# Kernel optimization log

Hardware: AMD Instinct MI355X
Metric: run time of the kernel (lower is better)

The kernel has to match this reference:

```python
import jax, jax.numpy as jnp
import numpy as np
from jax.ops import segment_sum

N_NODES = 50000
N_EDGES = 800000
D = 128
N_LAYERS = 3
N_GRAPHS = 256


def setup_inputs() -> dict:
    key = jax.random.key(0)
    k1, k2, k3, k4, k5, k6 = jax.random.split(key, 6)
    feats = jax.random.normal(k1, (N_NODES, D), dtype=jnp.float32)
    src = jax.random.randint(k2, (N_EDGES,), 0, N_NODES)
    dst = jax.random.randint(k3, (N_EDGES,), 0, N_NODES)
    graph_ids = jnp.sort(jax.random.randint(k4, (N_NODES,), 0, N_GRAPHS))
    W = jax.random.normal(k5, (N_LAYERS, D, D), dtype=jnp.float32) / np.float32(np.sqrt(D))
    b = jax.random.normal(k6, (N_LAYERS, D), dtype=jnp.float32) * 0.01
    return {"feats": feats, "W": W, "b": b, "src": src, "dst": dst, "graph_ids": graph_ids}


def reference(feats, W, b, src, dst, graph_ids):
    # DGL GraphConv with norm='both': h' = act(D_in^{-1/2} A D_out^{-1/2} h W + b)
    ones_e = jnp.ones((src.shape[0],), dtype=feats.dtype)
    deg_out = jnp.clip(segment_sum(ones_e, src, num_segments=N_NODES), 1.0)  # [N]
    deg_in = jnp.clip(segment_sum(ones_e, dst, num_segments=N_NODES), 1.0)   # [N]
    norm_out = jax.lax.rsqrt(deg_out)[:, None]  # [N,1]
    norm_in = jax.lax.rsqrt(deg_in)[:, None]    # [N,1]

    h = feats
    for l in range(N_LAYERS):
        hn = h * norm_out                                  # source-side norm
        agg = segment_sum(hn[src], dst, num_segments=N_NODES)  # SpMM gather/scatter
        agg = agg * norm_in                                # dest-side norm
        h = jax.nn.relu(agg @ W[l] + b[l])                 # [N,D]

    # AvgPooling readout: per-graph mean over nodes
    ones_n = jnp.ones((N_NODES,), dtype=h.dtype)
    counts = jnp.clip(segment_sum(ones_n, graph_ids, num_segments=N_GRAPHS), 1.0)
    pooled = segment_sum(h, graph_ids, num_segments=N_GRAPHS) / counts[:, None]
    return pooled  # [N_GRAPHS, D]
```

## Files before the change

kernel.cpp:

```cpp
#include <hip/hip_runtime.h>
#include <hip/hip_fp16.h>

#define DD 128
#define GG 256
#define RANGES 8
#define RSMAX 6400
#define NCHUNK 32

typedef _Float16 half8 __attribute__((ext_vector_type(8)));
typedef float floatx4 __attribute__((ext_vector_type(4)));

__device__ inline uint2 pack_half4(float4 v) {
    __half2 a = __floats2half2_rn(v.x, v.y);
    __half2 b = __floats2half2_rn(v.z, v.w);
    uint2 u;
    u.x = *reinterpret_cast<unsigned int*>(&a);
    u.y = *reinterpret_cast<unsigned int*>(&b);
    return u;
}

__global__ __launch_bounds__(256) void k_hist2(const int* __restrict__ src, const int* __restrict__ dst,
                                               unsigned int* __restrict__ pk,
                                               int E, int N, int C, int RS, int L) {
    __shared__ int ho[RSMAX];
    __shared__ int hi[RSMAX];
    int r = blockIdx.x / C;
    int c = blockIdx.x % C;
    int r0 = r * RS;
    int r1 = min(r0 + RS, N);
    int nb = r1 - r0;
    for (int i = threadIdx.x; i < nb; i += 256) { ho[i] = 0; hi[i] = 0; }
    __syncthreads();
    int e0 = c * L, e1 = min(e0 + L, E);
    for (int e = e0 + threadIdx.x * 4; e < e1; e += 1024) {
        if (e + 3 < e1) {
            int4 s4 = *(const int4*)&src[e];
            int4 d4 = *(const int4*)&dst[e];
            if (s4.x >= r0 && s4.x < r1) atomicAdd(&ho[s4.x - r0], 1);
            if (s4.y >= r0 && s4.y < r1) atomicAdd(&ho[s4.y - r0], 1);
            if (s4.z >= r0 && s4.z < r1) atomicAdd(&ho[s4.z - r0], 1);
            if (s4.w >= r0 && s4.w < r1) atomicAdd(&ho[s4.w - r0], 1);
            if (d4.x >= r0 && d4.x < r1) atomicAdd(&hi[d4.x - r0], 1);
            if (d4.y >= r0 && d4.y < r1) atomicAdd(&hi[d4.y - r0], 1);
            if (d4.z >= r0 && d4.z < r1) atomicAdd(&hi[d4.z - r0], 1);
            if (d4.w >= r0 && d4.w < r1) atomicAdd(&hi[d4.w - r0], 1);
        } else {
            for (int j = 0; j < 4 && e + j < e1; ++j) {
                int s = src[e + j], d = dst[e + j];
                if (s >= r0 && s < r1) atomicAdd(&ho[s - r0], 1);
                if (d >= r0 && d < r1) atomicAdd(&hi[d - r0], 1);
            }
        }
    }
    __syncthreads();
    for (int i = threadIdx.x; i < nb; i += 256)
        pk[(size_t)c * N + r0 + i] = (unsigned int)ho[i] | ((unsigned int)hi[i] << 16);
}

__global__ void k_reduce(const unsigned int* __restrict__ pk,
                         float* __restrict__ norm_out, float* __restrict__ norm_in,
                         int* __restrict__ deg_in, int N, int C) {
    int n = blockIdx.x * blockDim.x + threadIdx.x;
    if (n >= N) return;
    int so = 0, si = 0;
    for (int c = 0; c < C; ++c) {
        unsigned int v = pk[(size_t)c * N + n];
        so += (int)(v & 0xFFFFu);
        si += (int)(v >> 16);
    }
    norm_out[n] = rsqrtf(fmaxf((float)so, 1.0f));
    norm_in[n] = rsqrtf(fmaxf((float)si, 1.0f));
    deg_in[n] = si;
}

__global__ void k_base(const unsigned int* __restrict__ pk, const int* __restrict__ row_ptr,
                       int* __restrict__ base, int N, int C) {
    int n = blockIdx.x * blockDim.x + threadIdx.x;
    if (n >= N) return;
    int run = row_ptr[n];
    for (int c = 0; c < C; ++c) {
        int h = (int)(pk[(size_t)c * N + n] >> 16);
        base[(size_t)c * N + n] = run;
        run += h;
    }
}

__global__ void k_gstart(const int* __restrict__ gid, int* g_start, int N, int G) {
    int g = blockIdx.x * blockDim.x + threadIdx.x;
    if (g > G) return;
    int lo = 0, hi = N;
    while (lo < hi) {
        int mid = (lo + hi) >> 1;
        if (gid[mid] < g) lo = mid + 1; else hi = mid;
    }
    g_start[g] = lo;
}

__global__ __launch_bounds__(256) void k_scan_a(const int* __restrict__ deg, int* bsum, int n) {
    __shared__ int wsum[4];
    int base = blockIdx.x * 1024 + threadIdx.x * 4;
    int s = 0;
    #pragma unroll
    for (int j = 0; j < 4; ++j) s += (base + j < n) ? deg[base + j] : 0;
    #pragma unroll
    for (int off = 32; off; off >>= 1) s += __shfl_xor(s, off);
    int lane = threadIdx.x & 63, w = threadIdx.x >> 6;
    if (lane == 0) wsum[w] = s;
    __syncthreads();
    if (threadIdx.x == 0) bsum[blockIdx.x] = wsum[0] + wsum[1] + wsum[2] + wsum[3];
}

__global__ void k_scan_b(int* bsum, int nblk, int* row_ptr, int n) {
    int lane = threadIdx.x;
    int carry = 0;
    for (int base = 0; base < nblk; base += 64) {
        int i = base + lane;
        int v = (i < nblk) ? bsum[i] : 0;
        int s = v;
        #pragma unroll
        for (int off = 1; off < 64; off <<= 1) {
            int u = __shfl_up(s, off);
            if (lane >= off) s += u;
        }
        if (i < nblk) bsum[i] = carry + s - v;
        carry += __shfl(s, 63);
    }
    if (lane == 0) row_ptr[n] = carry;
}

__global__ __launch_bounds__(256) void k_scan_c(const int* __restrict__ deg, const int* __restrict__ bsum,
                                                int* row_ptr, int n) {
    __shared__ int wsum[4];
    int t = threadIdx.x;
    int base = blockIdx.x * 1024 + t * 4;
    int v[4];
    #pragma unroll
    for (int j = 0; j < 4; ++j) v[j] = (base + j < n) ? deg[base + j] : 0;
    int ts = v[0] + v[1] + v[2] + v[3];
    int lane = t & 63, w = t >> 6;
    int incl = ts;
    #pragma unroll
    for (int off = 1; off < 64; off <<= 1) {
        int u = __shfl_up(incl, off);
        if (lane >= off) incl += u;
    }
    if (lane == 63) wsum[w] = incl;
    __syncthreads();
    int woff = 0;
    for (int j = 0; j < w; ++j) woff += wsum[j];
    int run = bsum[blockIdx.x] + woff + incl - ts;
    #pragma unroll
    for (int j = 0; j < 4; ++j) {
        if (base + j < n) row_ptr[base + j] = run;
        run += v[j];
    }
}

__global__ __launch_bounds__(256) void k_fill2(const int* __restrict__ src, const int* __restrict__ dst,
                                               const int* __restrict__ base, int* __restrict__ col_src,
                                               int E, int N, int C, int RS, int L) {
    __shared__ int cnt[RSMAX];
    int r = blockIdx.x / C;
    int c = blockIdx.x % C;
    int r0 = r * RS;
    int r1 = min(r0 + RS, N);
    int nb = r1 - r0;
    const int* bc = base + (size_t)c * N;
    for (int i = threadIdx.x; i < nb; i += 256) cnt[i] = bc[r0 + i];
    __syncthreads();
    int e0 = c * L, e1 = min(e0 + L, E);
    for (int e = e0 + threadIdx.x * 4; e < e1; e += 1024) {
        if (e + 3 < e1) {
            int4 s4 = *(const int4*)&src[e];
            int4 d4 = *(const int4*)&dst[e];
            if (d4.x >= r0 && d4.x < r1) { int o = atomicAdd(&cnt[d4.x - r0], 1); col_src[o] = s4.x; }
            if (d4.y >= r0 && d4.y < r1) { int o = atomicAdd(&cnt[d4.y - r0], 1); col_src[o] = s4.y; }
            if (d4.z >= r0 && d4.z < r1) { int o = atomicAdd(&cnt[d4.z - r0], 1); col_src[o] = s4.z; }
            if (d4.w >= r0 && d4.w < r1) { int o = atomicAdd(&cnt[d4.w - r0], 1); col_src[o] = s4.w; }
        } else {
            for (int j = 0; j < 4 && e + j < e1; ++j) {
                int s = src[e + j], d = dst[e + j];
                if (d >= r0 && d < r1) { int o = atomicAdd(&cnt[d - r0], 1); col_src[o] = s; }
            }
        }
    }
}

__global__ void k_wconv(const float* __restrict__ W, __half* __restrict__ Wt) {
    int i = blockIdx.x * blockDim.x + threadIdx.x;
    if (i >= 3 * 16384) return;
    int l = i >> 14;
    int rem = i & 16383;
    int n = rem >> 7;
    int k = rem & 127;
    Wt[(size_t)l * 16384 + n * 128 + k] = __float2half(W[(size_t)l * 16384 + k * 128 + n]);
}

__global__ void k_scale(const float* __restrict__ h, const float* __restrict__ norm_out,
                        uint2* __restrict__ Xh, int N) {
    int i = blockIdx.x * blockDim.x + threadIdx.x;
    if (i < N * 32) {
        int n = i >> 5;
        float4 v = ((const float4*)h)[i];
        float s = norm_out[n];
        v.x *= s; v.y *= s; v.z *= s; v.w *= s;
        Xh[i] = pack_half4(v);
    }
}

__device__ inline void acc_row(float* acc, uint4 u) {
    const __half2* h = (const __half2*)&u;
    #pragma unroll
    for (int i = 0; i < 4; ++i) {
        float2 f = __half22float2(h[i]);
        acc[2 * i] += f.x;
        acc[2 * i + 1] += f.y;
    }
}

__global__ __launch_bounds__(256, 8) void k_agg(const uint4* __restrict__ Xin, const float* __restrict__ norm_in,
                                                const int* __restrict__ row_ptr, const int* __restrict__ col_src,
                                                uint4* __restrict__ Yh, int N) {
    int t = threadIdx.x;
    int l16 = t & 15;
    int n = blockIdx.x * 16 + (t >> 4);
    if (n >= N) return;
    int beg = row_ptr[n], end = row_ptr[n + 1];
    float acc[8] = {};
    int k = beg;
    bool have = (k + 3 < end);
    int4 s;
    if (have) s = *(const int4*)&col_src[k];
    while (have) {
        int kn = k + 4;
        bool haven = (kn + 3 < end);
        int4 sn = s;
        if (haven) sn = *(const int4*)&col_src[kn];
        uint4 u0 = Xin[(size_t)s.x * 16 + l16];
        uint4 u1 = Xin[(size_t)s.y * 16 + l16];
        uint4 u2 = Xin[(size_t)s.z * 16 + l16];
        uint4 u3 = Xin[(size_t)s.w * 16 + l16];
        acc_row(acc, u0);
        acc_row(acc, u1);
        acc_row(acc, u2);
        acc_row(acc, u3);
        s = sn; k = kn; have = haven;
    }
    for (; k < end; ++k) {
        uint4 u = Xin[(size_t)col_src[k] * 16 + l16];
        acc_row(acc, u);
    }
    float ni = norm_in[n];
    #pragma unroll
    for (int i = 0; i < 8; ++i) acc[i] *= ni;
    __half2 hp[4];
    #pragma unroll
    for (int i = 0; i < 4; ++i) hp[i] = __floats2half2_rn(acc[2 * i], acc[2 * i + 1]);
    Yh[(size_t)n * 16 + l16] = *(uint4*)hp;
}

__global__ __launch_bounds__(256) void k_mm_mfma(const __half* __restrict__ Yh, const __half* __restrict__ Wt,
                                                 const float* __restrict__ bl, const float* __restrict__ scale,
                                                 float* __restrict__ outf, __half* __restrict__ outh, int N) {
    __shared__ _Float16 Ah[64 * 136];
    __shared__ _Float16 Bt[128 * 136];
    int tid = threadIdx.x;
    int n0 = blockIdx.x * 64;

    for (int q = tid; q < 1024; q += 256) {
        int r = q >> 4, c = q & 15;
        int node = n0 + r;
        float4 v = make_float4(0.f, 0.f, 0.f, 0.f);
        if (node < N) v = *(const float4*)&Yh[(size_t)node * 128 + c * 8];
        *(float4*)&Ah[r * 136 + c * 8] = v;
    }
    for (int q = tid; q < 2048; q += 256) {
        int r = q >> 4, c = q & 15;
        *(float4*)&Bt[r * 136 + c * 8] = *(const float4*)&Wt[(size_t)r * 128 + c * 8];
    }
    __syncthreads();

    int wave = tid >> 6;
    int lane = tid & 63;
    int quad = lane >> 4;
    int mrow = lane & 15;
    int m0 = wave * 16;

    half8 af[4];
    #pragma unroll
    for (int kc = 0; kc < 4; ++kc)
        af[kc] = *(const half8*)&Ah[(m0 + mrow) * 136 + kc * 32 + quad * 8];

    floatx4 acc[8];
    #pragma unroll
    for (int ct = 0; ct < 8; ++ct) acc[ct] = (floatx4){0.f, 0.f, 0.f, 0.f};

    #pragma unroll
    for (int ct = 0; ct < 8; ++ct) {
        #pragma unroll
        for (int kc = 0; kc < 4; ++kc) {
            half8 bf = *(const half8*)&Bt[(ct * 16 + mrow) * 136 + kc * 32 + quad * 8];
            acc[ct] = __builtin_amdgcn_mfma_f32_16x16x32_f16(af[kc], bf, acc[ct], 0, 0, 0);
        }
    }

    float sc[4];
    #pragma unroll
    for (int r = 0; r < 4; ++r) {
        int node = n0 + m0 + quad * 4 + r;
        sc[r] = (scale && node < N) ? scale[node] : 1.0f;
    }
    #pragma unroll
    for (int ct = 0; ct < 8; ++ct) {
        int col = ct * 16 + mrow;
        float bias = bl[col];
        #pragma unroll
        for (int r = 0; r < 4; ++r) {
            int node = n0 + m0 + quad * 4 + r;
            if (node < N) {
                float val = fmaxf(acc[ct][r] + bias, 0.f);
                if (outh) outh[(size_t)node * 128 + col] = __float2half(val * sc[r]);
                else outf[(size_t)node * 128 + col] = val;
            }
        }
    }
}

__global__ __launch_bounds__(256) void k_pool(const __half2* __restrict__ Fh, const int* __restrict__ g_start,
                                              float* __restrict__ out) {
    __shared__ float2 red[4][64];
    int g = blockIdx.x;
    int t = threadIdx.x;
    int cp = t & 63;
    int nl = t >> 6;
    int beg = g_start[g], end = g_start[g + 1];
    float2 acc = make_float2(0.f, 0.f);
    for (int n = beg + nl; n < end; n += 4) {
        float2 f = __half22float2(Fh[(size_t)n * 64 + cp]);
        acc.x += f.x;
        acc.y += f.y;
    }
    red[nl][cp] = acc;
    __syncthreads();
    if (nl == 0) {
        float2 a0 = red[0][cp], a1 = red[1][cp], a2 = red[2][cp], a3 = red[3][cp];
        float cnt = fmaxf((float)(end - beg), 1.0f);
        float2 o;
        o.x = (a0.x + a1.x + a2.x + a3.x) / cnt;
        o.y = (a0.y + a1.y + a2.y + a3.y) / cnt;
        *(float2*)&out[(size_t)g * DD + cp * 2] = o;
    }
}

extern "C" void kernel_launch(void* const* d_in, const int* in_sizes, int n_in,
                              void* d_out, int out_size, void* d_ws, size_t ws_size,
                              hipStream_t stream) {
    const float* feats = (const float*)d_in[0];
    const float* W = (const float*)d_in[1];
    const float* b = (const float*)d_in[2];
    const int* src = (const int*)d_in[3];
    const int* dst = (const int*)d_in[4];
    const int* gid = (const int*)d_in[5];
    float* out = (float*)d_out;
    const int N = in_sizes[0] / DD;
    const int E = in_sizes[3];

    const int C = NCHUNK;
    const int RS = (N + RANGES - 1) / RANGES;
    const int L = (((E + C - 1) / C) + 3) & ~3;

    char* ws = (char*)d_ws;
    size_t off = 0;
    auto take = [&](size_t bytes) {
        char* p = ws + off;
        off = (off + bytes + 255) & ~(size_t)255;
        return p;
    };
    float* norm_out = (float*)take((size_t)N * 4);
    float* norm_in  = (float*)take((size_t)N * 4);
    int*   deg_in   = (int*)take((size_t)N * 4);
    int*   row_ptr  = (int*)take((size_t)(N + 1) * 4);
    int*   col_src  = (int*)take((size_t)E * 4);
    int*   g_start  = (int*)take((size_t)(GG + 1) * 4);
    int*   bsum     = (int*)take((size_t)1024 * 4);
    __half* Wth     = (__half*)take((size_t)3 * 16384 * 2);
    uint4* Xh       = (uint4*)take((size_t)N * DD * 2);
    uint4* Yh       = (uint4*)take((size_t)N * DD * 2);
    size_t chunk_arr = ((size_t)C * N * 4 + 255) & ~(size_t)255;
    size_t uni_bytes = 2 * chunk_arr;
    size_t fh_bytes = (size_t)N * DD * 2;
    char* uni = take(uni_bytes > fh_bytes ? uni_bytes : fh_bytes);
    unsigned int* pk = (unsigned int*)uni;
    int* fbase = (int*)(uni + chunk_arr);
    __half* Fh = (__half*)uni;

    const int nblk = (N + 1023) / 1024;

    k_hist2<<<RANGES * C, 256, 0, stream>>>(src, dst, pk, E, N, C, RS, L);
    k_reduce<<<(N + 255) / 256, 256, 0, stream>>>(pk, norm_out, norm_in, deg_in, N, C);
    k_gstart<<<1, 512, 0, stream>>>(gid, g_start, N, GG);
    k_wconv<<<(3 * 16384 + 255) / 256, 256, 0, stream>>>(W, Wth);
    k_scan_a<<<nblk, 256, 0, stream>>>(deg_in, bsum, N);
    k_scan_b<<<1, 64, 0, stream>>>(bsum, nblk, row_ptr, N);
    k_scan_c<<<nblk, 256, 0, stream>>>(deg_in, bsum, row_ptr, N);
    k_base<<<(N + 255) / 256, 256, 0, stream>>>(pk, row_ptr, fbase, N, C);
    k_fill2<<<RANGES * C, 256, 0, stream>>>(src, dst, fbase, col_src, E, N, C, RS, L);

    k_scale<<<(N * 32 + 255) / 256, 256, 0, stream>>>(feats, norm_out, (uint2*)Xh, N);

    const int agrid = (N + 15) / 16;
    const int mgrid = (N + 63) / 64;
    for (int l = 0; l < 3; ++l) {
        k_agg<<<agrid, 256, 0, stream>>>(Xh, norm_in, row_ptr, col_src, Yh, N);
        const __half* Wtl = Wth + (size_t)l * 16384;
        const float* bl = b + (size_t)l * DD;
        if (l < 2)
            k_mm_mfma<<<mgrid, 256, 0, stream>>>((const __half*)Yh, Wtl, bl, norm_out,
                                                 nullptr, (__half*)Xh, N);
        else
            k_mm_mfma<<<mgrid, 256, 0, stream>>>((const __half*)Yh, Wtl, bl, nullptr,
                                                 nullptr, Fh, N);
    }
    k_pool<<<GG, 256, 0, stream>>>((const __half2*)Fh, g_start, out);
}
```

Baseline: 313.5 us.

## Split degree histograms, fuse block sums into reduce, add nontemporal loads/stores

Result: slower. 340.5 us (+8.6%).

```diff
diff --git a/kernel.cpp b/kernel.cpp
--- a/kernel.cpp
+++ b/kernel.cpp
@@ -3,12 +3,14 @@
 
 #define DD 128
 #define GG 256
-#define RANGES 8
-#define RSMAX 6400
+#define RANGES 4
+#define RSMAX 12544
 #define NCHUNK 32
 
 typedef _Float16 half8 __attribute__((ext_vector_type(8)));
 typedef float floatx4 __attribute__((ext_vector_type(4)));
+typedef int intv4 __attribute__((ext_vector_type(4)));
+typedef unsigned int uintv4 __attribute__((ext_vector_type(4)));
 
 __device__ inline uint2 pack_half4(float4 v) {
     __half2 a = __floats2half2_rn(v.x, v.y);
@@ -19,95 +21,61 @@
     return u;
 }
 
-__global__ __launch_bounds__(256) void k_hist2(const int* __restrict__ src, const int* __restrict__ dst,
-                                               unsigned int* __restrict__ pk,
+__global__ __launch_bounds__(256) void k_hist1(const int* __restrict__ idx,
+                                               unsigned int* __restrict__ part,
                                                int E, int N, int C, int RS, int L) {
-    __shared__ int ho[RSMAX];
-    __shared__ int hi[RSMAX];
+    __shared__ int h[RSMAX];
     int r = blockIdx.x / C;
     int c = blockIdx.x % C;
     int r0 = r * RS;
     int r1 = min(r0 + RS, N);
     int nb = r1 - r0;
-    for (int i = threadIdx.x; i < nb; i += 256) { ho[i] = 0; hi[i] = 0; }
+    for (int i = threadIdx.x; i < nb; i += 256) h[i] = 0;
     __syncthreads();
     int e0 = c * L, e1 = min(e0 + L, E);
     for (int e = e0 + threadIdx.x * 4; e < e1; e += 1024) {
         if (e + 3 < e1) {
-            int4 s4 = *(const int4*)&src[e];
-            int4 d4 = *(const int4*)&dst[e];
-            if (s4.x >= r0 && s4.x < r1) atomicAdd(&ho[s4.x - r0], 1);
-            if (s4.y >= r0 && s4.y < r1) atomicAdd(&ho[s4.y - r0], 1);
-            if (s4.z >= r0 && s4.z < r1) atomicAdd(&ho[s4.z - r0], 1);
-            if (s4.w >= r0 && s4.w < r1) atomicAdd(&ho[s4.w - r0], 1);
-            if (d4.x >= r0 && d4.x < r1) atomicAdd(&hi[d4.x - r0], 1);
-            if (d4.y >= r0 && d4.y < r1) atomicAdd(&hi[d4.y - r0], 1);
-            if (d4.z >= r0 && d4.z < r1) atomicAdd(&hi[d4.z - r0], 1);
-            if (d4.w >= r0 && d4.w < r1) atomicAdd(&hi[d4.w - r0], 1);
+            int4 s4 = *(const int4*)&idx[e];
+            if (s4.x >= r0 && s4.x < r1) atomicAdd(&h[s4.x - r0], 1);
+            if (s4.y >= r0 && s4.y < r1) atomicAdd(&h[s4.y - r0], 1);
+            if (s4.z >= r0 && s4.z < r1) atomicAdd(&h[s4.z - r0], 1);
+            if (s4.w >= r0 && s4.w < r1) atomicAdd(&h[s4.w - r0], 1);
         } else {
             for (int j = 0; j < 4 && e + j < e1; ++j) {
-                int s = src[e + j], d = dst[e + j];
-                if (s >= r0 && s < r1) atomicAdd(&ho[s - r0], 1);
-                if (d >= r0 && d < r1) atomicAdd(&hi[d - r0], 1);
+                int s = idx[e + j];
+                if (s >= r0 && s < r1) atomicAdd(&h[s - r0], 1);
             }
         }
     }
     __syncthreads();
     for (int i = threadIdx.x; i < nb; i += 256)
-        pk[(size_t)c * N + r0 + i] = (unsigned int)ho[i] | ((unsigned int)hi[i] << 16);
-}
-
-__global__ void k_reduce(const unsigned int* __restrict__ pk,
-                         float* __restrict__ norm_out, float* __restrict__ norm_in,
-                         int* __restrict__ deg_in, int N, int C) {
-    int n = blockIdx.x * blockDim.x + threadIdx.x;
-    if (n >= N) return;
+        part[(size_t)c * N + r0 + i] = (unsigned int)h[i];
+}
+
+__global__ __launch_bounds__(256) void k_reduce(const unsigned int* __restrict__ pout,
+                                                const unsigned int* __restrict__ pin,
+                                                float* __restrict__ norm_out, float* __restrict__ norm_in,
+                                                int* __restrict__ deg_in, int* __restrict__ bsum,
+                                                int N, int C) {
+    __shared__ int ws[4];
+    int n = blockIdx.x * 256 + threadIdx.x;
     int so = 0, si = 0;
-    for (int c = 0; c < C; ++c) {
-        unsigned int v = pk[(size_t)c * N + n];
-        so += (int)(v & 0xFFFFu);
-        si += (int)(v >> 16);
-    }
-    norm_out[n] = rsqrtf(fmaxf((float)so, 1.0f));
-    norm_in[n] = rsqrtf(fmaxf((float)si, 1.0f));
-    deg_in[n] = si;
-}
-
-__global__ void k_base(const unsigned int* __restrict__ pk, const int* __restrict__ row_ptr,
-                       int* __restrict__ base, int N, int C) {
-    int n = blockIdx.x * blockDim.x + threadIdx.x;
-    if (n >= N) return;
-    int run = row_ptr[n];
-    for (int c = 0; c < C; ++c) {
-        int h = (int)(pk[(size_t)c * N + n] >> 16);
-        base[(size_t)c * N + n] = run;
-        run += h;
-    }
-}
-
-__global__ void k_gstart(const int* __restrict__ gid, int* g_start, int N, int G) {
-    int g = blockIdx.x * blockDim.x + threadIdx.x;
-    if (g > G) return;
-    int lo = 0, hi = N;
-    while (lo < hi) {
-        int mid = (lo + hi) >> 1;
-        if (gid[mid] < g) lo = mid + 1; else hi = mid;
-    }
-    g_start[g] = lo;
-}
-
-__global__ __launch_bounds__(256) void k_scan_a(const int* __restrict__ deg, int* bsum, int n) {
-    __shared__ int wsum[4];
-    int base = blockIdx.x * 1024 + threadIdx.x * 4;
-    int s = 0;
-    #pragma unroll
-    for (int j = 0; j < 4; ++j) s += (base + j < n) ? deg[base + j] : 0;
+    if (n < N) {
+        for (int c = 0; c < C; ++c) {
+            so += (int)pout[(size_t)c * N + n];
+            si += (int)pin[(size_t)c * N + n];
+        }
+        norm_out[n] = rsqrtf(fmaxf((float)so, 1.0f));
+        norm_in[n] = rsqrtf(fmaxf((float)si, 1.0f));
+        deg_in[n] = si;
+    }
+    int s = si;
     #pragma unroll
     for (int off = 32; off; off >>= 1) s += __shfl_xor(s, off);
     int lane = threadIdx.x & 63, w = threadIdx.x >> 6;
-    if (lane == 0) wsum[w] = s;
-    __syncthreads();
-    if (threadIdx.x == 0) bsum[blockIdx.x] = wsum[0] + wsum[1] + wsum[2] + wsum[3];
+    if (lane == 0) ws[w] = s;
+    __syncthreads();
+    if (threadIdx.x == 0) bsum[blockIdx.x] = ws[0] + ws[1] + ws[2] + ws[3];
 }
 
 __global__ void k_scan_b(int* bsum, int nblk, int* row_ptr, int n) {
@@ -129,31 +97,46 @@
 }
 
 __global__ __launch_bounds__(256) void k_scan_c(const int* __restrict__ deg, const int* __restrict__ bsum,
-                                                int* row_ptr, int n) {
-    __shared__ int wsum[4];
+                                                int* __restrict__ row_ptr, int N) {
+    __shared__ int ws[4];
     int t = threadIdx.x;
-    int base = blockIdx.x * 1024 + t * 4;
-    int v[4];
-    #pragma unroll
-    for (int j = 0; j < 4; ++j) v[j] = (base + j < n) ? deg[base + j] : 0;
-    int ts = v[0] + v[1] + v[2] + v[3];
+    int n = blockIdx.x * 256 + t;
+    int v = (n < N) ? deg[n] : 0;
     int lane = t & 63, w = t >> 6;
-    int incl = ts;
+    int incl = v;
     #pragma unroll
     for (int off = 1; off < 64; off <<= 1) {
         int u = __shfl_up(incl, off);
         if (lane >= off) incl += u;
     }
-    if (lane == 63) wsum[w] = incl;
+    if (lane == 63) ws[w] = incl;
     __syncthreads();
     int woff = 0;
-    for (int j = 0; j < w; ++j) woff += wsum[j];
-    int run = bsum[blockIdx.x] + woff + incl - ts;
-    #pragma unroll
-    for (int j = 0; j < 4; ++j) {
-        if (base + j < n) row_ptr[base + j] = run;
-        run += v[j];
-    }
+    for (int j = 0; j < w; ++j) woff += ws[j];
+    if (n < N) row_ptr[n] = bsum[blockIdx.x] + woff + incl - v;
+}
+
+__global__ void k_base(const unsigned int* __restrict__ pin, const int* __restrict__ row_ptr,
+                       int* __restrict__ base, int N, int C) {
+    int n = blockIdx.x * blockDim.x + threadIdx.x;
+    if (n >= N) return;
+    int run = row_ptr[n];
+    for (int c = 0; c < C; ++c) {
+        int h = (int)pin[(size_t)c * N + n];
+        base[(size_t)c * N + n] = run;
+        run += h;
+    }
+}
+
+__global__ void k_gstart(const int* __restrict__ gid, int* g_start, int N, int G) {
+    int g = blockIdx.x * blockDim.x + threadIdx.x;
+    if (g > G) return;
+    int lo = 0, hi = N;
+    while (lo < hi) {
+        int mid = (lo + hi) >> 1;
+        if (gid[mid] < g) lo = mid + 1; else hi = mid;
+    }
+    g_start[g] = lo;
 }
 
 __global__ __launch_bounds__(256) void k_fill2(const int* __restrict__ src, const int* __restrict__ dst,
@@ -229,13 +212,13 @@
     float acc[8] = {};
     int k = beg;
     bool have = (k + 3 < end);
-    int4 s;
-    if (have) s = *(const int4*)&col_src[k];
+    intv4 s = {0, 0, 0, 0};
+    if (have) s = __builtin_nontemporal_load((const intv4*)&col_src[k]);
     while (have) {
         int kn = k + 4;
         bool haven = (kn + 3 < end);
-        int4 sn = s;
-        if (haven) sn = *(const int4*)&col_src[kn];
+        intv4 sn = s;
+        if (haven) sn = __builtin_nontemporal_load((const intv4*)&col_src[kn]);
         uint4 u0 = Xin[(size_t)s.x * 16 + l16];
         uint4 u1 = Xin[(size_t)s.y * 16 + l16];
         uint4 u2 = Xin[(size_t)s.z * 16 + l16];
@@ -256,7 +239,7 @@
     __half2 hp[4];
     #pragma unroll
     for (int i = 0; i < 4; ++i) hp[i] = __floats2half2_rn(acc[2 * i], acc[2 * i + 1]);
-    Yh[(size_t)n * 16 + l16] = *(uint4*)hp;
+    __builtin_nontemporal_store(*(uintv4*)hp, (uintv4*)&Yh[(size_t)n * 16 + l16]);
 }
 
 __global__ __launch_bounds__(256) void k_mm_mfma(const __half* __restrict__ Yh, const __half* __restrict__ Wt,
@@ -270,9 +253,9 @@
     for (int q = tid; q < 1024; q += 256) {
         int r = q >> 4, c = q & 15;
         int node = n0 + r;
-        float4 v = make_float4(0.f, 0.f, 0.f, 0.f);
-        if (node < N) v = *(const float4*)&Yh[(size_t)node * 128 + c * 8];
-        *(float4*)&Ah[r * 136 + c * 8] = v;
+        floatx4 v = {0.f, 0.f, 0.f, 0.f};
+        if (node < N) v = __builtin_nontemporal_load((const floatx4*)&Yh[(size_t)node * 128 + c * 8]);
+        *(floatx4*)&Ah[r * 136 + c * 8] = v;
     }
     for (int q = tid; q < 2048; q += 256) {
         int r = q >> 4, c = q & 15;
@@ -387,23 +370,24 @@
     uint4* Xh       = (uint4*)take((size_t)N * DD * 2);
     uint4* Yh       = (uint4*)take((size_t)N * DD * 2);
     size_t chunk_arr = ((size_t)C * N * 4 + 255) & ~(size_t)255;
-    size_t uni_bytes = 2 * chunk_arr;
+    size_t uni_bytes = 3 * chunk_arr;
     size_t fh_bytes = (size_t)N * DD * 2;
     char* uni = take(uni_bytes > fh_bytes ? uni_bytes : fh_bytes);
-    unsigned int* pk = (unsigned int*)uni;
-    int* fbase = (int*)(uni + chunk_arr);
+    unsigned int* pout = (unsigned int*)uni;
+    unsigned int* pin  = (unsigned int*)(uni + chunk_arr);
+    int* fbase = (int*)(uni + 2 * chunk_arr);
     __half* Fh = (__half*)uni;
 
-    const int nblk = (N + 1023) / 1024;
-
-    k_hist2<<<RANGES * C, 256, 0, stream>>>(src, dst, pk, E, N, C, RS, L);
-    k_reduce<<<(N + 255) / 256, 256, 0, stream>>>(pk, norm_out, norm_in, deg_in, N, C);
+    const int nblk = (N + 255) / 256;
+
+    k_hist1<<<RANGES * C, 256, 0, stream>>>(src, pout, E, N, C, RS, L);
+    k_hist1<<<RANGES * C, 256, 0, stream>>>(dst, pin, E, N, C, RS, L);
+    k_reduce<<<nblk, 256, 0, stream>>>(pout, pin, norm_out, norm_in, deg_in, bsum, N, C);
     k_gstart<<<1, 512, 0, stream>>>(gid, g_start, N, GG);
     k_wconv<<<(3 * 16384 + 255) / 256, 256, 0, stream>>>(W, Wth);
-    k_scan_a<<<nblk, 256, 0, stream>>>(deg_in, bsum, N);
     k_scan_b<<<1, 64, 0, stream>>>(bsum, nblk, row_ptr, N);
     k_scan_c<<<nblk, 256, 0, stream>>>(deg_in, bsum, row_ptr, N);
-    k_base<<<(N + 255) / 256, 256, 0, stream>>>(pk, row_ptr, fbase, N, C);
+    k_base<<<(N + 255) / 256, 256, 0, stream>>>(pin, row_ptr, fbase, N, C);
     k_fill2<<<RANGES * C, 256, 0, stream>>>(src, dst, fbase, col_src, E, N, C, RS, L);
 
     k_scale<<<(N * 32 + 255) / 256, 256, 0, stream>>>(feats, norm_out, (uint2*)Xh, N);
```
